# Kernel tuning notes

Hardware: AMD Instinct MI355X
Metric: run time of the kernel (lower is better)

The kernel has to match this reference:

```python
import jax, jax.numpy as jnp
import numpy as np

B, K, I, H = 32768, 4, 256, 256


def _linear_init(key, out_dim, in_dim, bias):
    # mimics torch nn.Linear default init: U(-1/sqrt(in), 1/sqrt(in))
    bound = 1.0 / np.sqrt(in_dim)
    kw, kb = jax.random.split(key)
    W = jax.random.uniform(kw, (out_dim, in_dim), minval=-bound, maxval=bound, dtype=jnp.float32)
    if bias:
        b = jax.random.uniform(kb, (out_dim,), minval=-bound, maxval=bound, dtype=jnp.float32)
        return W, b
    return W


def setup_inputs() -> dict:
    key = jax.random.key(0)
    ks = jax.random.split(key, 12)
    x = jax.random.normal(ks[0], (B, I), dtype=jnp.float32)
    child_x = jax.random.normal(ks[1], (B, K, I), dtype=jnp.float32)
    Wi, bi = _linear_init(ks[2], H, I, True)
    Wf, bf = _linear_init(ks[3], H, I, True)
    Wo, bo = _linear_init(ks[4], H, I, True)
    Wu, bu = _linear_init(ks[5], H, I, True)
    Ui = _linear_init(ks[6], H, H, False)
    Uo = _linear_init(ks[7], H, H, False)
    Uu = _linear_init(ks[8], H, H, False)
    # per-arity forget weights wf1..wfK, stacked [K, H, H]
    WfK = jnp.stack([_linear_init(jax.random.fold_in(ks[9], k), H, H, False) for k in range(K)])
    return dict(x=x, child_x=child_x, Wi=Wi, bi=bi, Wf=Wf, bf=bf, Wo=Wo, bo=bo,
                Wu=Wu, bu=bu, Ui=Ui, Uo=Uo, Uu=Uu, WfK=WfK)


def reference(x, child_x, Wi, bi, Wf, bf, Wo, bo, Wu, bu, Ui, Uo, Uu, WfK):
    # ---- leaf_forward on all K children, batched: [B, K, H] ----
    ci = jax.nn.sigmoid(child_x @ Wi.T + bi)
    co = jax.nn.sigmoid(child_x @ Wo.T + bo)
    cu = jnp.tanh(child_x @ Wu.T + bu)
    cc = ci * cu                      # child cell states [B, K, H]
    ch = co * jnp.tanh(cc)            # child hidden states [B, K, H]

    # ---- node_forward on root ----
    hsum = ch.sum(axis=1)             # sum_j h_j  [B, H]
    i = jax.nn.sigmoid(x @ Wi.T + bi + hsum @ Ui.T)
    # faithful quirk: f_k = sigmoid(Wf x + Wf_k @ (sum_j h_j))
    ukfh = jnp.einsum('bh,kgh->bkg', hsum, WfK)                 # [B, K, H]
    f = jax.nn.sigmoid((x @ Wf.T + bf)[:, None, :] + ukfh)       # [B, K, H]
    o = jax.nn.sigmoid(x @ Wo.T + bo + hsum @ Uo.T)
    u = jnp.tanh(x @ Wu.T + bu + hsum @ Uu.T)
    c = i * u + (f * cc).sum(axis=1)  # [B, H]
    h = o * jnp.tanh(c)
    return (h, c)
```

## Files before the change

### kernel.cpp

```cpp
#include <hip/hip_runtime.h>
#include <hip/hip_bf16.h>


#define BB 32768
#define KK 4
#define II 256
#define HH 256

typedef __bf16 bf16x8 __attribute__((ext_vector_type(8)));
typedef __bf16 bf16x4 __attribute__((ext_vector_type(4)));
typedef float f32x4 __attribute__((ext_vector_type(4)));

#define MFMA16(a, b, c) __builtin_amdgcn_mfma_f32_16x16x32_bf16(a, b, c, 0, 0, 0)

static __device__ __forceinline__ float fsig(float x) {
    return 1.0f / (1.0f + __expf(-x));
}
static __device__ __forceinline__ float ftanhf(float x) {
    float e = __expf(2.0f * x);
    return 1.0f - 2.0f / (e + 1.0f);
}

static __device__ __forceinline__ bf16x8 cvt8v(float4 f0, float4 f1) {
    bf16x8 v;
    v[0] = (__bf16)f0.x; v[1] = (__bf16)f0.y; v[2] = (__bf16)f0.z; v[3] = (__bf16)f0.w;
    v[4] = (__bf16)f1.x; v[5] = (__bf16)f1.y; v[6] = (__bf16)f1.z; v[7] = (__bf16)f1.w;
    return v;
}
static __device__ __forceinline__ bf16x8 cvt8(const float* __restrict__ p) {
    return cvt8v(((const float4*)p)[0], ((const float4*)p)[1]);
}

struct CvtArgs {
    const float* src[8];
    __bf16* dst[8];
    int n[8];
};
__global__ __launch_bounds__(256) void cvt_k(CvtArgs a) {
    const int t = blockIdx.y;
    const int i = (blockIdx.x * 256 + threadIdx.x) * 4;
    if (i < a.n[t]) {
        float4 f = *(const float4*)(a.src[t] + i);
        bf16x4 v;
        v[0] = (__bf16)f.x; v[1] = (__bf16)f.y; v[2] = (__bf16)f.z; v[3] = (__bf16)f.w;
        *(bf16x4*)(a.dst[t] + i) = v;
    }
}

#define ROWSTR 264
__global__ __launch_bounds__(512, 2) void child_gates_k(
    const float* __restrict__ child_x,
    const __bf16* __restrict__ Wi, const __bf16* __restrict__ Wo,
    const __bf16* __restrict__ Wu,
    const float* __restrict__ bi, const float* __restrict__ bo,
    const float* __restrict__ bu,
    __bf16* __restrict__ cc, __bf16* __restrict__ hsum)
{
    const int tid  = threadIdx.x;
    const int wave = tid >> 6;
    const int lane = tid & 63;
    const int l16  = lane & 15;
    const int quad = lane >> 4;
    const int rowchunk = blockIdx.x >> 1;
    const int ct   = (blockIdx.x & 1) * 8 + wave;
    const int n    = ct * 16 + l16;

    bf16x8 w[3][8];
    {
        const int base = n * II + quad * 8;
#pragma unroll
        for (int ks = 0; ks < 8; ++ks) {
            w[0][ks] = *(const bf16x8*)(Wi + base + ks * 32);
            w[1][ks] = *(const bf16x8*)(Wo + base + ks * 32);
            w[2][ks] = *(const bf16x8*)(Wu + base + ks * 32);
        }
    }
    const float bin = bi[n], bon = bo[n], bun = bu[n];

    __shared__ __bf16 As[2][16 * ROWSTR];

    const int srow = tid >> 5;
    const int scol = (tid & 31) * 8;
    const float* gbase = child_x + ((size_t)rowchunk * 256 + srow) * II + scol;

    float4 f0 = ((const float4*)gbase)[0];
    float4 f1 = ((const float4*)gbase)[1];
    *(bf16x8*)(&As[0][srow * ROWSTR + scol]) = cvt8v(f0, f1);
    __syncthreads();

    for (int t = 0; t < 16; ++t) {
        float4 g0, g1;
        if (t < 15) {
            const float* gp = gbase + (size_t)(t + 1) * 16 * II;
            g0 = ((const float4*)gp)[0];
            g1 = ((const float4*)gp)[1];
        }

        const __bf16* ap = &As[t & 1][l16 * ROWSTR + quad * 8];
        f32x4 ai = {0.f,0.f,0.f,0.f}, ao = {0.f,0.f,0.f,0.f}, au = {0.f,0.f,0.f,0.f};
#pragma unroll
        for (int ks = 0; ks < 8; ++ks) {
            bf16x8 a = *(const bf16x8*)(ap + ks * 32);
            ai = MFMA16(a, w[0][ks], ai);
            ao = MFMA16(a, w[1][ks], ao);
            au = MFMA16(a, w[2][ks], au);
        }

        {
            const int b = rowchunk * 64 + t * 4 + quad;
            float chs = 0.f;
            bf16x4 ccv4;
#pragma unroll
            for (int r = 0; r < 4; ++r) {
                float civ = fsig(ai[r] + bin);
                float cov = fsig(ao[r] + bon);
                float cuv = ftanhf(au[r] + bun);
                float ccv = civ * cuv;
                chs += cov * ftanhf(ccv);
                ccv4[r] = (__bf16)ccv;
            }
            *(bf16x4*)(cc + ((size_t)b * HH + n) * KK) = ccv4;
            hsum[(size_t)b * HH + n] = (__bf16)chs;
        }

        if (t < 15)
            *(bf16x8*)(&As[(t + 1) & 1][srow * ROWSTR + scol]) = cvt8v(g0, g1);
        __syncthreads();
    }
}

__global__ __launch_bounds__(256, 2) void root_k(
    const float* __restrict__ x,
    const __bf16* __restrict__ Wi, const __bf16* __restrict__ Wf,
    const __bf16* __restrict__ Wo, const __bf16* __restrict__ Wu,
    const __bf16* __restrict__ Ui, const __bf16* __restrict__ Uo,
    const __bf16* __restrict__ Uu, const __bf16* __restrict__ WfK,
    const float* __restrict__ bi, const float* __restrict__ bf_,
    const float* __restrict__ bo, const float* __restrict__ bu,
    const __bf16* __restrict__ cc, const __bf16* __restrict__ hsum,
    float* __restrict__ out)
{
    const int lane = threadIdx.x & 63;
    const int wave = threadIdx.x >> 6;
    const int l16  = lane & 15;
    const int quad = lane >> 4;
    const int rbase = blockIdx.x * 128 + wave * 32;
    const int ctbase = blockIdx.y * 8;

    bf16x8 ax[2][8], ah[2][8];
#pragma unroll
    for (int t = 0; t < 2; ++t) {
        const float*  xp = x    + (size_t)(rbase + t * 16 + l16) * II + quad * 8;
        const __bf16* hp = hsum + (size_t)(rbase + t * 16 + l16) * HH + quad * 8;
#pragma unroll
        for (int ks = 0; ks < 8; ++ks) {
            ax[t][ks] = cvt8(xp + ks * 32);
            ah[t][ks] = *(const bf16x8*)(hp + ks * 32);
        }
    }

    for (int ctl = 0; ctl < 8; ++ctl) {
        const int n = (ctbase + ctl) * 16 + l16;
        const float bin = bi[n], bfn = bf_[n], bon = bo[n], bun = bu[n];
        const int wo = n * II + quad * 8;

        f32x4 ai[2] = {{0.f,0.f,0.f,0.f},{0.f,0.f,0.f,0.f}};
        f32x4 ao[2] = {{0.f,0.f,0.f,0.f},{0.f,0.f,0.f,0.f}};
        f32x4 au[2] = {{0.f,0.f,0.f,0.f},{0.f,0.f,0.f,0.f}};
#pragma unroll
        for (int ks = 0; ks < 8; ++ks) {
            const int o = wo + ks * 32;
            bf16x8 bwi = *(const bf16x8*)(Wi + o);
            bf16x8 bui = *(const bf16x8*)(Ui + o);
            bf16x8 bwo = *(const bf16x8*)(Wo + o);
            bf16x8 buo = *(const bf16x8*)(Uo + o);
            bf16x8 bwu = *(const bf16x8*)(Wu + o);
            bf16x8 buu = *(const bf16x8*)(Uu + o);
#pragma unroll
            for (int t = 0; t < 2; ++t) {
                ai[t] = MFMA16(ax[t][ks], bwi, ai[t]);
                ai[t] = MFMA16(ah[t][ks], bui, ai[t]);
                ao[t] = MFMA16(ax[t][ks], bwo, ao[t]);
                ao[t] = MFMA16(ah[t][ks], buo, ao[t]);
                au[t] = MFMA16(ax[t][ks], bwu, au[t]);
                au[t] = MFMA16(ah[t][ks], buu, au[t]);
            }
        }
        float iv[2][4], ov[2][4], uv[2][4];
#pragma unroll
        for (int t = 0; t < 2; ++t)
#pragma unroll
            for (int r = 0; r < 4; ++r) {
                iv[t][r] = fsig(ai[t][r] + bin);
                ov[t][r] = fsig(ao[t][r] + bon);
                uv[t][r] = ftanhf(au[t][r] + bun);
            }

        f32x4 axf[2] = {{0.f,0.f,0.f,0.f},{0.f,0.f,0.f,0.f}};
        f32x4 af[4][2] = {{{0.f,0.f,0.f,0.f},{0.f,0.f,0.f,0.f}},
                          {{0.f,0.f,0.f,0.f},{0.f,0.f,0.f,0.f}},
                          {{0.f,0.f,0.f,0.f},{0.f,0.f,0.f,0.f}},
                          {{0.f,0.f,0.f,0.f},{0.f,0.f,0.f,0.f}}};
#pragma unroll
        for (int ks = 0; ks < 8; ++ks) {
            const int o = wo + ks * 32;
            bf16x8 bwf = *(const bf16x8*)(Wf + o);
            bf16x8 bk0 = *(const bf16x8*)(WfK + 0 * HH * II + o);
            bf16x8 bk1 = *(const bf16x8*)(WfK + 1 * HH * II + o);
            bf16x8 bk2 = *(const bf16x8*)(WfK + 2 * HH * II + o);
            bf16x8 bk3 = *(const bf16x8*)(WfK + 3 * HH * II + o);
#pragma unroll
            for (int t = 0; t < 2; ++t) {
                axf[t]   = MFMA16(ax[t][ks], bwf, axf[t]);
                af[0][t] = MFMA16(ah[t][ks], bk0, af[0][t]);
                af[1][t] = MFMA16(ah[t][ks], bk1, af[1][t]);
                af[2][t] = MFMA16(ah[t][ks], bk2, af[2][t]);
                af[3][t] = MFMA16(ah[t][ks], bk3, af[3][t]);
            }
        }

#pragma unroll
        for (int t = 0; t < 2; ++t)
#pragma unroll
            for (int r = 0; r < 4; ++r) {
                const int b = rbase + t * 16 + quad * 4 + r;
                bf16x4 cv4 = *(const bf16x4*)(cc + ((size_t)b * HH + n) * KK);
                const float xfv = axf[t][r] + bfn;
                float cv = iv[t][r] * uv[t][r];
#pragma unroll
                for (int k = 0; k < 4; ++k)
                    cv += fsig(xfv + af[k][t][r]) * (float)cv4[k];
                float hv = ov[t][r] * ftanhf(cv);
                out[(size_t)b * HH + n] = hv;
                out[(size_t)BB * HH + (size_t)b * HH + n] = cv;
            }
    }
}

extern "C" void kernel_launch(void* const* d_in, const int* in_sizes, int n_in,
                              void* d_out, int out_size, void* d_ws, size_t ws_size,
                              hipStream_t stream) {
    const float* x    = (const float*)d_in[0];
    const float* cx   = (const float*)d_in[1];
    const float* Wi   = (const float*)d_in[2];
    const float* bi   = (const float*)d_in[3];
    const float* Wf   = (const float*)d_in[4];
    const float* bf_  = (const float*)d_in[5];
    const float* Wo   = (const float*)d_in[6];
    const float* bo   = (const float*)d_in[7];
    const float* Wu   = (const float*)d_in[8];
    const float* bu   = (const float*)d_in[9];
    const float* Ui   = (const float*)d_in[10];
    const float* Uo   = (const float*)d_in[11];
    const float* Uu   = (const float*)d_in[12];
    const float* WfK  = (const float*)d_in[13];

    __bf16* cc = (__bf16*)d_ws;
    __bf16* hs = cc + (size_t)BB * KK * HH;
    __bf16* wb = hs + (size_t)BB * HH;
    __bf16 *Wi_b = wb,            *Wf_b = Wi_b + HH * II, *Wo_b = Wf_b + HH * II,
           *Wu_b = Wo_b + HH * II, *Ui_b = Wu_b + HH * II, *Uo_b = Ui_b + HH * HH,
           *Uu_b = Uo_b + HH * HH, *WfK_b = Uu_b + HH * HH;

    CvtArgs ca;
    ca.src[0] = Wi;  ca.dst[0] = Wi_b;  ca.n[0] = HH * II;
    ca.src[1] = Wf;  ca.dst[1] = Wf_b;  ca.n[1] = HH * II;
    ca.src[2] = Wo;  ca.dst[2] = Wo_b;  ca.n[2] = HH * II;
    ca.src[3] = Wu;  ca.dst[3] = Wu_b;  ca.n[3] = HH * II;
    ca.src[4] = Ui;  ca.dst[4] = Ui_b;  ca.n[4] = HH * HH;
    ca.src[5] = Uo;  ca.dst[5] = Uo_b;  ca.n[5] = HH * HH;
    ca.src[6] = Uu;  ca.dst[6] = Uu_b;  ca.n[6] = HH * HH;
    ca.src[7] = WfK; ca.dst[7] = WfK_b; ca.n[7] = KK * HH * HH;

    cvt_k<<<dim3(KK * HH * HH / 1024, 8), dim3(256), 0, stream>>>(ca);
    child_gates_k<<<dim3(1024), dim3(512), 0, stream>>>(
        cx, Wi_b, Wo_b, Wu_b, bi, bo, bu, cc, hs);
    root_k<<<dim3(BB / 128, 2), dim3(256), 0, stream>>>(
        x, Wi_b, Wf_b, Wo_b, Wu_b, Ui_b, Uo_b, Uu_b, WfK_b,
        bi, bf_, bo, bu, cc, hs, (float*)d_out);
}
```

Baseline: 601.2 us.

## Stage root activations in swizzled LDS and give each wave one column tile

The root kernel now loads a 64-row tile of x (converted to bf16) and hsum into XOR-swizzled shared memory once per block. Each wave then computes one 16-column output tile over all 64 rows. Before, each wave held its 32 rows in registers and looped over 8 column tiles. This cuts redundant global weight reads per row and the register pressure from holding activations. The cost is 64 KB of LDS per block, which may limit occupancy, and x/hsum being reloaded by four times as many column blocks.

```diff
diff --git a/kernel.cpp b/kernel.cpp
--- a/kernel.cpp
+++ b/kernel.cpp
@@ -140,67 +140,113 @@
     const __bf16* __restrict__ cc, const __bf16* __restrict__ hsum,
     float* __restrict__ out)
 {
-    const int lane = threadIdx.x & 63;
-    const int wave = threadIdx.x >> 6;
+    const int tid  = threadIdx.x;
+    const int lane = tid & 63;
+    const int wave = tid >> 6;
     const int l16  = lane & 15;
     const int quad = lane >> 4;
-    const int rbase = blockIdx.x * 128 + wave * 32;
-    const int ctbase = blockIdx.y * 8;
-
-    bf16x8 ax[2][8], ah[2][8];
-#pragma unroll
-    for (int t = 0; t < 2; ++t) {
-        const float*  xp = x    + (size_t)(rbase + t * 16 + l16) * II + quad * 8;
-        const __bf16* hp = hsum + (size_t)(rbase + t * 16 + l16) * HH + quad * 8;
-#pragma unroll
-        for (int ks = 0; ks < 8; ++ks) {
-            ax[t][ks] = cvt8(xp + ks * 32);
-            ah[t][ks] = *(const bf16x8*)(hp + ks * 32);
-        }
-    }
-
-    for (int ctl = 0; ctl < 8; ++ctl) {
-        const int n = (ctbase + ctl) * 16 + l16;
-        const float bin = bi[n], bfn = bf_[n], bon = bo[n], bun = bu[n];
-        const int wo = n * II + quad * 8;
-
-        f32x4 ai[2] = {{0.f,0.f,0.f,0.f},{0.f,0.f,0.f,0.f}};
-        f32x4 ao[2] = {{0.f,0.f,0.f,0.f},{0.f,0.f,0.f,0.f}};
-        f32x4 au[2] = {{0.f,0.f,0.f,0.f},{0.f,0.f,0.f,0.f}};
-#pragma unroll
-        for (int ks = 0; ks < 8; ++ks) {
-            const int o = wo + ks * 32;
-            bf16x8 bwi = *(const bf16x8*)(Wi + o);
-            bf16x8 bui = *(const bf16x8*)(Ui + o);
-            bf16x8 bwo = *(const bf16x8*)(Wo + o);
-            bf16x8 buo = *(const bf16x8*)(Uo + o);
-            bf16x8 bwu = *(const bf16x8*)(Wu + o);
-            bf16x8 buu = *(const bf16x8*)(Uu + o);
-#pragma unroll
-            for (int t = 0; t < 2; ++t) {
-                ai[t] = MFMA16(ax[t][ks], bwi, ai[t]);
-                ai[t] = MFMA16(ah[t][ks], bui, ai[t]);
-                ao[t] = MFMA16(ax[t][ks], bwo, ao[t]);
-                ao[t] = MFMA16(ah[t][ks], buo, ao[t]);
-                au[t] = MFMA16(ax[t][ks], bwu, au[t]);
-                au[t] = MFMA16(ah[t][ks], buu, au[t]);
-            }
-        }
-        float iv[2][4], ov[2][4], uv[2][4];
-#pragma unroll
-        for (int t = 0; t < 2; ++t)
+    const int row0 = blockIdx.x * 64;
+    const int ct   = blockIdx.y * 4 + wave;
+    const int n    = ct * 16 + l16;
+
+    __shared__ __bf16 xs[64 * 256];
+    __shared__ __bf16 hsl[64 * 256];
+
+    {
+        const float* xg = x + (size_t)row0 * II;
+#pragma unroll
+        for (int p = 0; p < 16; ++p) {
+            const int e = p * 1024 + tid * 4;
+            float4 f = *(const float4*)(xg + e);
+            bf16x4 v;
+            v[0] = (__bf16)f.x; v[1] = (__bf16)f.y;
+            v[2] = (__bf16)f.z; v[3] = (__bf16)f.w;
+            const int r = e >> 8, c = e & 255;
+            int off = r * 512 + c * 2;
+            off ^= (r & 7) << 4;
+            *(bf16x4*)((char*)xs + off) = v;
+        }
+        const __bf16* hg = hsum + (size_t)row0 * HH;
+#pragma unroll
+        for (int p = 0; p < 8; ++p) {
+            const int u = p * 256 + tid;
+            bf16x8 v = *(const bf16x8*)(hg + u * 8);
+            const int r = u >> 5, c = (u & 31) * 8;
+            int off = r * 512 + c * 2;
+            off ^= (r & 7) << 4;
+            *(bf16x8*)((char*)hsl + off) = v;
+        }
+    }
+    __syncthreads();
+
+    const float bin = bi[n], bfn = bf_[n], bon = bo[n], bun = bu[n];
+    const int wo = n * II + quad * 8;
+    const int cbase = quad * 8;
+
+#define LDA(plane, rt, ks) \
+    (*(const bf16x8*)((const char*)(plane) + \
+        ((((rt) * 16 + l16) * 512 + ((cbase) + (ks) * 32) * 2) ^ \
+         ((((rt) * 16 + l16) & 7) << 4))))
+
+    f32x4 ai[4], ao[4], au[4];
+    {
+        const f32x4 z = {0.f, 0.f, 0.f, 0.f};
+#pragma unroll
+        for (int rt = 0; rt < 4; ++rt) { ai[rt] = z; ao[rt] = z; au[rt] = z; }
+    }
+#pragma unroll
+    for (int ks = 0; ks < 8; ++ks) {
+        const int o = wo + ks * 32;
+        bf16x8 bwi = *(const bf16x8*)(Wi + o);
+        bf16x8 bui = *(const bf16x8*)(Ui + o);
+        bf16x8 bwo = *(const bf16x8*)(Wo + o);
+        bf16x8 buo = *(const bf16x8*)(Uo + o);
+        bf16x8 bwu = *(const bf16x8*)(Wu + o);
+        bf16x8 buu = *(const bf16x8*)(Uu + o);
+#pragma unroll
+        for (int rt = 0; rt < 4; ++rt) {
+            bf16x8 a = LDA(xs, rt, ks);
+            bf16x8 h = LDA(hsl, rt, ks);
+            ai[rt] = MFMA16(a, bwi, ai[rt]);
+            ai[rt] = MFMA16(h, bui, ai[rt]);
+            ao[rt] = MFMA16(a, bwo, ao[rt]);
+            ao[rt] = MFMA16(h, buo, ao[rt]);
+            au[rt] = MFMA16(a, bwu, au[rt]);
+            au[rt] = MFMA16(h, buu, au[rt]);
+        }
+    }
+    f32x4 cpart[4], ovv[4];
+#pragma unroll
+    for (int rt = 0; rt < 4; ++rt)
+#pragma unroll
+        for (int r = 0; r < 4; ++r) {
+            const float iv = fsig(ai[rt][r] + bin);
+            const float ov = fsig(ao[rt][r] + bon);
+            const float uv = ftanhf(au[rt][r] + bun);
+            cpart[rt][r] = iv * uv;
+            ovv[rt][r]   = ov;
+        }
+
+#pragma unroll
+    for (int h2 = 0; h2 < 2; ++h2) {
+        bf16x4 cv4[2][4];
+#pragma unroll
+        for (int rt2 = 0; rt2 < 2; ++rt2)
 #pragma unroll
             for (int r = 0; r < 4; ++r) {
-                iv[t][r] = fsig(ai[t][r] + bin);
-                ov[t][r] = fsig(ao[t][r] + bon);
-                uv[t][r] = ftanhf(au[t][r] + bun);
-            }
-
-        f32x4 axf[2] = {{0.f,0.f,0.f,0.f},{0.f,0.f,0.f,0.f}};
-        f32x4 af[4][2] = {{{0.f,0.f,0.f,0.f},{0.f,0.f,0.f,0.f}},
-                          {{0.f,0.f,0.f,0.f},{0.f,0.f,0.f,0.f}},
-                          {{0.f,0.f,0.f,0.f},{0.f,0.f,0.f,0.f}},
-                          {{0.f,0.f,0.f,0.f},{0.f,0.f,0.f,0.f}}};
+                const int b = row0 + (h2 * 2 + rt2) * 16 + quad * 4 + r;
+                cv4[rt2][r] = *(const bf16x4*)(cc + ((size_t)b * HH + n) * KK);
+            }
+
+        f32x4 axf[2], af0[2], af1[2], af2[2], af3[2];
+        {
+            const f32x4 z = {0.f, 0.f, 0.f, 0.f};
+#pragma unroll
+            for (int rt2 = 0; rt2 < 2; ++rt2) {
+                axf[rt2] = z; af0[rt2] = z; af1[rt2] = z;
+                af2[rt2] = z; af3[rt2] = z;
+            }
+        }
 #pragma unroll
         for (int ks = 0; ks < 8; ++ks) {
             const int o = wo + ks * 32;
@@ -210,31 +256,37 @@
             bf16x8 bk2 = *(const bf16x8*)(WfK + 2 * HH * II + o);
             bf16x8 bk3 = *(const bf16x8*)(WfK + 3 * HH * II + o);
 #pragma unroll
-            for (int t = 0; t < 2; ++t) {
-                axf[t]   = MFMA16(ax[t][ks], bwf, axf[t]);
-                af[0][t] = MFMA16(ah[t][ks], bk0, af[0][t]);
-                af[1][t] = MFMA16(ah[t][ks], bk1, af[1][t]);
-                af[2][t] = MFMA16(ah[t][ks], bk2, af[2][t]);
-                af[3][t] = MFMA16(ah[t][ks], bk3, af[3][t]);
-            }
-        }
-
-#pragma unroll
-        for (int t = 0; t < 2; ++t)
+            for (int rt2 = 0; rt2 < 2; ++rt2) {
+                const int rt = h2 * 2 + rt2;
+                bf16x8 a = LDA(xs, rt, ks);
+                bf16x8 h = LDA(hsl, rt, ks);
+                axf[rt2] = MFMA16(a, bwf, axf[rt2]);
+                af0[rt2] = MFMA16(h, bk0, af0[rt2]);
+                af1[rt2] = MFMA16(h, bk1, af1[rt2]);
+                af2[rt2] = MFMA16(h, bk2, af2[rt2]);
+                af3[rt2] = MFMA16(h, bk3, af3[rt2]);
+            }
+        }
+
+#pragma unroll
+        for (int rt2 = 0; rt2 < 2; ++rt2) {
+            const int rt = h2 * 2 + rt2;
 #pragma unroll
             for (int r = 0; r < 4; ++r) {
-                const int b = rbase + t * 16 + quad * 4 + r;
-                bf16x4 cv4 = *(const bf16x4*)(cc + ((size_t)b * HH + n) * KK);
-                const float xfv = axf[t][r] + bfn;
-                float cv = iv[t][r] * uv[t][r];
-#pragma unroll
-                for (int k = 0; k < 4; ++k)
-                    cv += fsig(xfv + af[k][t][r]) * (float)cv4[k];
-                float hv = ov[t][r] * ftanhf(cv);
+                const int b = row0 + rt * 16 + quad * 4 + r;
+                const float xfv = axf[rt2][r] + bfn;
+                float cv = cpart[rt][r];
+                cv += fsig(xfv + af0[rt2][r]) * (float)cv4[rt2][r][0];
+                cv += fsig(xfv + af1[rt2][r]) * (float)cv4[rt2][r][1];
+                cv += fsig(xfv + af2[rt2][r]) * (float)cv4[rt2][r][2];
+                cv += fsig(xfv + af3[rt2][r]) * (float)cv4[rt2][r][3];
+                const float hv = ovv[rt][r] * ftanhf(cv);
                 out[(size_t)b * HH + n] = hv;
                 out[(size_t)BB * HH + (size_t)b * HH + n] = cv;
             }
-    }
+        }
+    }
+#undef LDA
 }
 
 extern "C" void kernel_launch(void* const* d_in, const int* in_sizes, int n_in,
@@ -275,7 +327,7 @@
     cvt_k<<<dim3(KK * HH * HH / 1024, 8), dim3(256), 0, stream>>>(ca);
     child_gates_k<<<dim3(1024), dim3(512), 0, stream>>>(
         cx, Wi_b, Wo_b, Wu_b, bi, bo, bu, cc, hs);
-    root_k<<<dim3(BB / 128, 2), dim3(256), 0, stream>>>(
+    root_k<<<dim3(BB / 64, 4), dim3(256), 0, stream>>>(
         x, Wi_b, Wf_b, Wo_b, Wu_b, Ui_b, Uo_b, Uu_b, WfK_b,
         bi, bf_, bo, bu, cc, hs, (float*)d_out);
 }
```

Measured after the change: 493.5 us. -17.9%, faster.
